# Performance work log

Hardware: AMD Instinct MI355X
Metric: run time of the kernel (lower is better)

## Reference

```python
import jax, jax.numpy as jnp
import numpy as np

N_QUBITS = 12
LAYERS = 8
N_CLASS = 10
BATCH = 2048
FEAT = 3072  # CIFAR-10 flattened 3*32*32
DIM = 2 ** N_QUBITS


def _apply_ry_layer(psi, angles):
    """Apply Ry(angles[q]) to qubit q for all q. psi: [B, 2,...,2] complex.
    kron order in the torch code makes qubit 0 the MSB -> tensor axis q+1."""
    c, s = jnp.cos(angles), jnp.sin(angles)
    for q in range(N_QUBITS):
        rot = jnp.stack([jnp.stack([c[q], -s[q]]), jnp.stack([s[q], c[q]])]).astype(psi.dtype)
        # contract qubit axis with rot (rows index output): psi'[..a..] = rot[a,b] psi[..b..]
        psi = jnp.moveaxis(jnp.tensordot(psi, rot, axes=([q + 1], [1])), -1, q + 1)
    return psi


def _cnot(psi, control, target):
    """CNOT == proj0(c) x I(t) + proj1(c) x X(t): flip target bit where control bit is 1."""
    ca, ta = control + 1, target + 1
    flipped = jnp.flip(psi, axis=ta)          # X on target qubit
    p0 = jax.lax.index_in_dim(psi, 0, axis=ca, keepdims=True)      # control = 0: identity
    p1 = jax.lax.index_in_dim(flipped, 1, axis=ca, keepdims=True)  # control = 1: X
    return jnp.concatenate([p0, p1], axis=ca)


def setup_inputs() -> dict:
    key = jax.random.key(0)
    kx, ka, kw = jax.random.split(key, 3)
    x = jax.random.normal(kx, (BATCH, FEAT), dtype=jnp.float32)
    angles = jax.random.uniform(ka, (LAYERS, N_QUBITS), minval=-0.01, maxval=0.01, dtype=jnp.float32)
    W = jax.random.normal(kw, (N_CLASS, DIM), dtype=jnp.float32) * np.float32(1.0 / np.sqrt(DIM))
    b = jnp.zeros((N_CLASS,), dtype=jnp.float32)
    return {"x": x, "angles": angles, "W": W, "b": b}


def reference(x, angles, W, b):
    B = x.shape[0]
    # CIFAR branch: right-pad features to 2^n, flatten (no-op for 2D), L2-normalize rows
    x = jnp.pad(x, ((0, 0), (0, DIM - x.shape[1])))
    x = x / jnp.linalg.norm(x, axis=1, keepdims=True)
    psi = x.astype(jnp.complex64).reshape((B,) + (2,) * N_QUBITS)
    for l in range(LAYERS):
        psi = _apply_ry_layer(psi, angles[l])
        # cx_linear_layer: CNOT(n-2,n-1), then CNOT(i,i+1) for i = n-3..0
        psi = _cnot(psi, N_QUBITS - 2, N_QUBITS - 1)
        for i in range(N_QUBITS - 3, -1, -1):
            psi = _cnot(psi, i, i + 1)
    probs = (psi.real ** 2 + psi.imag ** 2).reshape(B, DIM)  # Re(conj(psi)*psi)
    return probs @ W.T + b
```

## Files before the change

kernel.cpp:

```cpp
#include <hip/hip_runtime.h>
#include <math.h>

#define LAYERS  8
#define FEAT    3072
#define NCLASS  10
#define DIM     4096
#define ST      68
#define SBF     (ST * 64)

typedef float v2f __attribute__((ext_vector_type(2)));
typedef float v4f __attribute__((ext_vector_type(4)));

__device__ __forceinline__ int px6c(int r) {
    int u = r ^ (r >> 1); u ^= u >> 2; u ^= u >> 4; return u & 63;
}
__device__ __forceinline__ int gray6(int r) { return (r ^ (r >> 1)) & 63; }

__device__ __forceinline__ float getc(const v2f v[32], int u) {
    return (u & 1) ? v[u >> 1].y : v[u >> 1].x;
}
__device__ __forceinline__ void setc(v2f v[32], int u, float x) {
    if (u & 1) v[u >> 1].y = x; else v[u >> 1].x = x;
}
__device__ __forceinline__ float bpermf(int addr, float x) {
    return __int_as_float(__builtin_amdgcn_ds_bpermute(addr, __float_as_int(x)));
}

__device__ __forceinline__ void butterflies6(v2f v[32],
                                             const float* __restrict__ cl,
                                             const float* __restrict__ sl,
                                             int off) {
    {
        const float c = cl[off], s = sl[off];
        const v2f c2 = {c, c};
        const v2f ms = {-s, s};
#pragma unroll
        for (int i = 0; i < 32; ++i) {
            v2f a = v[i];
            v2f sw = {a.y, a.x};
            v[i] = a * c2 + sw * ms;
        }
    }
#pragma unroll
    for (int p = 1; p < 6; ++p) {
        const float c = cl[off - p], s = sl[off - p];
        const v2f c2 = {c, c};
        const v2f s2 = {s, s};
#pragma unroll
        for (int i0 = 0; i0 < 32; ++i0) {
            if (i0 & (1 << (p - 1))) continue;
            const int i1 = i0 | (1 << (p - 1));
            v2f a = v[i0], e = v[i1];
            v[i0] = a * c2 - e * s2;
            v[i1] = a * s2 + e * c2;
        }
    }
}

__device__ __forceinline__ void butterflies6_renamed(v2f v[32],
                                                     const float* __restrict__ cl,
                                                     const float* __restrict__ sl,
                                                     float psgn) {
    {
        const float c = cl[11], s = sl[11];
        const v2f c2 = {c, c};
        const v2f msA = {-s, s};
        const v2f msB = {s, -s};
#pragma unroll
        for (int k = 0; k < 32; ++k) {
            v2f a = v[k];
            v2f sw = {a.y, a.x};
            v[k] = a * c2 + sw * ((k & 1) ? msB : msA);
        }
    }
#pragma unroll
    for (int b = 1; b < 5; ++b) {
        const float c = cl[11 - b], s = sl[11 - b];
        const v2f c2 = {c, c};
#pragma unroll
        for (int m = 0; m < 32; ++m) {
            if (m & (1 << (b - 1))) continue;
            const int part = m ^ ((1 << b) - 1);
            const float sg = (m & (1 << b)) ? -s : s;
            const v2f sg2 = {sg, sg};
            const v2f A = v[m], E = v[part];
            const v2f Esw = {E.y, E.x};
            const v2f Asw = {A.y, A.x};
            v[m]    = A * c2 - Esw * sg2;
            v[part] = Asw * sg2 + E * c2;
        }
    }
    {
        const float c = cl[6];
        const float snl = psgn * sl[6];
        const v2f c2 = {c, c};
        const v2f sg2 = {snl, snl};
#pragma unroll
        for (int m = 0; m < 16; ++m) {
            const int part = m ^ 31;
            const v2f A = v[m], E = v[part];
            const v2f Esw = {E.y, E.x};
            const v2f Asw = {A.y, A.x};
            v[m]    = A * c2 - Esw * sg2;
            v[part] = Asw * sg2 + E * c2;
        }
    }
}

__global__ __launch_bounds__(64, 1)
void qnn_kernel(const float* __restrict__ x,
                const float* __restrict__ ang,
                const float* __restrict__ W,
                const float* __restrict__ bias,
                float* __restrict__ out,
                int batch)
{
    __shared__ __attribute__((aligned(16))) float lds[2 * SBF];
    __shared__ float cst[96], snt[96];

    const int t = threadIdx.x;
    const int b = blockIdx.x;
    const int b0 = 2 * b, b1 = 2 * b + 1;
    const bool has1 = (b1 < batch);

    {
        float a0 = ang[t];
        cst[t] = cosf(a0);
        snt[t] = sinf(a0);
        if (t < 32) {
            float a1 = ang[64 + t];
            cst[64 + t] = cosf(a1);
            snt[64 + t] = sinf(a1);
        }
    }

    v2f v0[32], v1[32];
    {
        const float* xb = x + (size_t)b0 * FEAT;
#pragma unroll
        for (int r = 0; r < 64; ++r) {
            if (r < FEAT / 64) setc(v0, r, xb[64 * r + t]);
            else               setc(v0, r, 0.f);
        }
    }
    if (has1) {
        const float* xb = x + (size_t)b1 * FEAT;
#pragma unroll
        for (int r = 0; r < 64; ++r) {
            if (r < FEAT / 64) setc(v1, r, xb[64 * r + t]);
            else               setc(v1, r, 0.f);
        }
    } else {
#pragma unroll
        for (int i = 0; i < 32; ++i) v1[i] = (v2f){0.f, 0.f};
    }

    float invn0, invn1;
    {
        v2f s2 = {0.f, 0.f};
#pragma unroll
        for (int i = 0; i < 32; ++i) s2 += v0[i] * v0[i];
        float ss = s2.x + s2.y;
#pragma unroll
        for (int o = 1; o < 64; o <<= 1) ss += __shfl_xor(ss, o, 64);
        invn0 = 1.0f / ss;
    }
    {
        v2f s2 = {0.f, 0.f};
#pragma unroll
        for (int i = 0; i < 32; ++i) s2 += v1[i] * v1[i];
        float ss = s2.x + s2.y;
#pragma unroll
        for (int o = 1; o < 64; o <<= 1) ss += __shfl_xor(ss, o, 64);
        invn1 = 1.0f / ss;
    }

    {
        const int slot = __builtin_amdgcn_s_getreg(4 | (4 << 6) | (1 << 11)) & 3;
#pragma unroll 1
        for (int i = 0; i < slot; ++i) __builtin_amdgcn_s_sleep(12);
    }

    int px = t ^ (t >> 1); px ^= px >> 2; px ^= px >> 4; px &= 63;
    const int A0 = 4 * px;
    const int A1 = 4 * (px ^ 63);
    const int u0 = t & 1;
    const float psgn = u0 ? -1.f : 1.f;
    const int gtl = gray6(t);
    const int bp  = gtl + 32 * ST * u0;
    const int bm  = gtl - 32 * ST * u0;

    auto storeRows = [&](const v2f* vv, const int SB) {
#pragma unroll
        for (int i = 0; i < 16; ++i) {
            v4f q = {vv[2 * i].x, vv[2 * i].y, vv[2 * i + 1].x, vv[2 * i + 1].y};
            *(v4f*)(lds + SB + ST * t + 4 * i) = q;
        }
    };
    auto readCols = [&](v2f* vv, const int SB) {
#pragma unroll
        for (int u = 0; u < 64; ++u)
            setc(vv, u, lds[SB + t + ST * u]);
    };
    auto foldedStore = [&](const v2f* vv, const int SB) {
#pragma unroll
        for (int s = 0; s < 64; ++s) {
            const int g = gray6(s);
            lds[SB + ((g & 32) ? bm : bp) + ST * g] = getc(vv, s);
        }
    };
    auto rowRead = [&](v2f* vv, const int SB) {
#pragma unroll
        for (int i = 0; i < 16; ++i) {
            v4f q = *(const v4f*)(lds + SB + ST * t + 4 * i);
            vv[2 * i]     = (v2f){q.x, q.y};
            vv[2 * i + 1] = (v2f){q.z, q.w};
        }
    };
    auto grayB = [&](v2f* vv) {
        float n[64];
#pragma unroll
        for (int r = 0; r < 64; ++r) {
            const int srcr = px6c(r);
            n[r] = bpermf((srcr & 1) ? A1 : A0, getc(vv, srcr));
        }
#pragma unroll
        for (int r = 0; r < 64; ++r) setc(vv, r, n[r]);
    };

    {
        const float* cl = cst;
        const float* sl = snt;
        butterflies6(v0, cl, sl, 5);
        butterflies6(v1, cl, sl, 5);
        storeRows(v0, 0);  storeRows(v1, SBF);
        readCols(v0, 0);   readCols(v1, SBF);
        butterflies6(v0, cl, sl, 11);
        butterflies6(v1, cl, sl, 11);
    }

#pragma unroll 1
    for (int p = 0; p < 4; ++p) {
        {
            const float* cl = cst + (2 * p + 1) * 12;
            const float* sl = snt + (2 * p + 1) * 12;

            butterflies6_renamed(v0, cl, sl, psgn);
            butterflies6_renamed(v1, cl, sl, psgn);
            foldedStore(v0, 0);  foldedStore(v1, SBF);
            rowRead(v0, 0);      rowRead(v1, SBF);
            butterflies6(v0, cl, sl, 5);
            butterflies6(v1, cl, sl, 5);

            if (p < 3) {
                grayB(v0);
                grayB(v1);
            }
        }

        if (p == 3) break;

        {
            const float* cl = cst + (2 * p + 2) * 12;
            const float* sl = snt + (2 * p + 2) * 12;

            butterflies6(v0, cl, sl, 5);
            butterflies6(v1, cl, sl, 5);
            storeRows(v0, 0);  storeRows(v1, SBF);
            readCols(v0, 0);   readCols(v1, SBF);
            butterflies6(v0, cl, sl, 11);
            butterflies6(v1, cl, sl, 11);
        }
    }

#pragma unroll
    for (int i = 0; i < 32; ++i) {
        const int g0 = 64 * gray6(2 * i);
        const int g1 = 64 * (gray6(2 * i) ^ 1);
        lds[g0 + gtl]        = v0[i].x * v0[i].x;
        lds[g1 + (gtl ^ 32)] = v0[i].y * v0[i].y;
        lds[SBF + g0 + gtl]        = v1[i].x * v1[i].x;
        lds[SBF + g1 + (gtl ^ 32)] = v1[i].y * v1[i].y;
    }

    float acc0[NCLASS], acc1[NCLASS];
#pragma unroll
    for (int c = 0; c < NCLASS; ++c) { acc0[c] = 0.f; acc1[c] = 0.f; }

#pragma unroll 1
    for (int k = 0; k < 16; ++k) {
        const v4f qa = *(const v4f*)(lds + 4 * t + 256 * k);
        const v4f qb = *(const v4f*)(lds + SBF + 4 * t + 256 * k);
        const float* wp = W + 4 * t + 256 * k;
#pragma unroll
        for (int c = 0; c < NCLASS; ++c) {
            const v4f w4 = *(const v4f*)(wp + c * DIM);
            acc0[c] += qa.x * w4.x + qa.y * w4.y + qa.z * w4.z + qa.w * w4.w;
            acc1[c] += qb.x * w4.x + qb.y * w4.y + qb.z * w4.z + qb.w * w4.w;
        }
    }

#pragma unroll
    for (int c = 0; c < NCLASS; ++c) {
        float a0 = acc0[c], a1 = acc1[c];
#pragma unroll
        for (int o = 1; o < 64; o <<= 1) {
            a0 += __shfl_xor(a0, o, 64);
            a1 += __shfl_xor(a1, o, 64);
        }
        if (t == 0) {
            out[b0 * NCLASS + c] = fmaf(a0, invn0, bias[c]);
            if (has1) out[b1 * NCLASS + c] = fmaf(a1, invn1, bias[c]);
        }
    }
}

extern "C" void kernel_launch(void* const* d_in, const int* in_sizes, int n_in,
                              void* d_out, int out_size, void* d_ws, size_t ws_size,
                              hipStream_t stream) {
    const float* x    = (const float*)d_in[0];
    const float* ang  = (const float*)d_in[1];
    const float* W    = (const float*)d_in[2];
    const float* bias = (const float*)d_in[3];
    float* out = (float*)d_out;
    const int batch = in_sizes[0] / FEAT;
    const int blocks = (batch + 1) / 2;
    qnn_kernel<<<blocks, 64, 0, stream>>>(x, ang, W, bias, out, batch);
}
```

Before: 122.2 us.

## Interleave LDS transposes of one state with butterflies of the other via packed FMA

Rewrites the butterfly stages with inline-asm v_pk_mul/v_pk_fma (including op_sel swap variants) so each complex rotation becomes one packed mul plus one packed fma. The two batch states' stages are then software-interleaved: LDS stores, reads and bpermute chunks for one state are issued alongside butterfly stages of the other. This is meant to hide LDS and cross-lane latency behind ALU work in a single-wave block. It raises register pressure (n0/n1 arrays live together), and inline asm limits compiler scheduling.

Result: slower. 131.3 us (+7.4%).

```diff
diff --git a/kernel.cpp b/kernel.cpp
--- a/kernel.cpp
+++ b/kernel.cpp
@@ -26,85 +26,73 @@
     return __int_as_float(__builtin_amdgcn_ds_bpermute(addr, __float_as_int(x)));
 }
 
-__device__ __forceinline__ void butterflies6(v2f v[32],
-                                             const float* __restrict__ cl,
-                                             const float* __restrict__ sl,
-                                             int off) {
-    {
-        const float c = cl[off], s = sl[off];
-        const v2f c2 = {c, c};
-        const v2f ms = {-s, s};
-#pragma unroll
-        for (int i = 0; i < 32; ++i) {
-            v2f a = v[i];
-            v2f sw = {a.y, a.x};
-            v[i] = a * c2 + sw * ms;
-        }
-    }
-#pragma unroll
-    for (int p = 1; p < 6; ++p) {
-        const float c = cl[off - p], s = sl[off - p];
-        const v2f c2 = {c, c};
-        const v2f s2 = {s, s};
-#pragma unroll
-        for (int i0 = 0; i0 < 32; ++i0) {
-            if (i0 & (1 << (p - 1))) continue;
-            const int i1 = i0 | (1 << (p - 1));
-            v2f a = v[i0], e = v[i1];
-            v[i0] = a * c2 - e * s2;
-            v[i1] = a * s2 + e * c2;
-        }
-    }
-}
-
-__device__ __forceinline__ void butterflies6_renamed(v2f v[32],
-                                                     const float* __restrict__ cl,
-                                                     const float* __restrict__ sl,
-                                                     float psgn) {
-    {
-        const float c = cl[11], s = sl[11];
-        const v2f c2 = {c, c};
-        const v2f msA = {-s, s};
-        const v2f msB = {s, -s};
-#pragma unroll
-        for (int k = 0; k < 32; ++k) {
-            v2f a = v[k];
-            v2f sw = {a.y, a.x};
-            v[k] = a * c2 + sw * ((k & 1) ? msB : msA);
-        }
-    }
-#pragma unroll
-    for (int b = 1; b < 5; ++b) {
-        const float c = cl[11 - b], s = sl[11 - b];
-        const v2f c2 = {c, c};
-#pragma unroll
-        for (int m = 0; m < 32; ++m) {
-            if (m & (1 << (b - 1))) continue;
-            const int part = m ^ ((1 << b) - 1);
-            const float sg = (m & (1 << b)) ? -s : s;
-            const v2f sg2 = {sg, sg};
-            const v2f A = v[m], E = v[part];
-            const v2f Esw = {E.y, E.x};
-            const v2f Asw = {A.y, A.x};
-            v[m]    = A * c2 - Esw * sg2;
-            v[part] = Asw * sg2 + E * c2;
-        }
-    }
-    {
-        const float c = cl[6];
-        const float snl = psgn * sl[6];
-        const v2f c2 = {c, c};
-        const v2f sg2 = {snl, snl};
-#pragma unroll
-        for (int m = 0; m < 16; ++m) {
-            const int part = m ^ 31;
-            const v2f A = v[m], E = v[part];
-            const v2f Esw = {E.y, E.x};
-            const v2f Asw = {A.y, A.x};
-            v[m]    = A * c2 - Esw * sg2;
-            v[part] = Asw * sg2 + E * c2;
-        }
-    }
+__device__ __forceinline__ v2f pk_mul(v2f a, v2f b) {
+    v2f d; asm("v_pk_mul_f32 %0, %1, %2" : "=v"(d) : "v"(a), "v"(b)); return d;
+}
+__device__ __forceinline__ v2f pk_fma(v2f a, v2f b, v2f c) {
+    v2f d; asm("v_pk_fma_f32 %0, %1, %2, %3" : "=v"(d) : "v"(a), "v"(b), "v"(c)); return d;
+}
+__device__ __forceinline__ v2f pk_fma_swap(v2f a, v2f b, v2f c) {
+    v2f d; asm("v_pk_fma_f32 %0, %1, %2, %3 op_sel:[1,0,0] op_sel_hi:[0,1,1]"
+               : "=v"(d) : "v"(a), "v"(b), "v"(c));
+    return d;
+}
+
+__device__ __forceinline__ void bf_s0(v2f v[32], float c, float s) {
+    const v2f c2 = {c, c}, ms = {-s, s};
+#pragma unroll
+    for (int i = 0; i < 32; ++i) {
+        v2f a = v[i];
+        v[i] = pk_fma_swap(a, ms, pk_mul(a, c2));
+    }
+}
+__device__ __forceinline__ void bf_sp(v2f v[32], int p, float c, float s) {
+    const v2f c2 = {c, c}, s2 = {s, s}, ns2 = {-s, -s};
+#pragma unroll
+    for (int i0 = 0; i0 < 32; ++i0) {
+        if (i0 & (1 << (p - 1))) continue;
+        const int i1 = i0 | (1 << (p - 1));
+        v2f a = v[i0], e = v[i1];
+        v[i0] = pk_fma(e, ns2, pk_mul(a, c2));
+        v[i1] = pk_fma(a, s2,  pk_mul(e, c2));
+    }
+}
+__device__ __forceinline__ void bfr_s0(v2f v[32], float c, float s) {
+    const v2f c2 = {c, c}, msA = {-s, s}, msB = {s, -s};
+#pragma unroll
+    for (int k = 0; k < 32; ++k) {
+        v2f a = v[k];
+        v[k] = pk_fma_swap(a, (k & 1) ? msB : msA, pk_mul(a, c2));
+    }
+}
+__device__ __forceinline__ void bfr_sb(v2f v[32], int b, float c, float s) {
+    const v2f c2 = {c, c};
+#pragma unroll
+    for (int m = 0; m < 32; ++m) {
+        if (m & (1 << (b - 1))) continue;
+        const int part = m ^ ((1 << b) - 1);
+        const float sg = (m & (1 << b)) ? -s : s;
+        const v2f sg2 = {sg, sg}, nsg2 = {-sg, -sg};
+        v2f A = v[m], E = v[part];
+        v[m]    = pk_fma_swap(E, nsg2, pk_mul(A, c2));
+        v[part] = pk_fma_swap(A, sg2,  pk_mul(E, c2));
+    }
+}
+__device__ __forceinline__ void bfr_s5(v2f v[32], float c, float snl) {
+    const v2f c2 = {c, c}, sg2 = {snl, snl}, nsg2 = {-snl, -snl};
+#pragma unroll
+    for (int m = 0; m < 16; ++m) {
+        const int part = m ^ 31;
+        v2f A = v[m], E = v[part];
+        v[m]    = pk_fma_swap(E, nsg2, pk_mul(A, c2));
+        v[part] = pk_fma_swap(A, sg2,  pk_mul(E, c2));
+    }
+}
+__device__ __forceinline__ void bf6_full(v2f v[32], const float* __restrict__ cl,
+                                         const float* __restrict__ sl, int off) {
+    bf_s0(v, cl[off], sl[off]);
+#pragma unroll
+    for (int p = 1; p < 6; ++p) bf_sp(v, p, cl[off - p], sl[off - p]);
 }
 
 __global__ __launch_bounds__(64, 1)
@@ -159,7 +147,7 @@
     {
         v2f s2 = {0.f, 0.f};
 #pragma unroll
-        for (int i = 0; i < 32; ++i) s2 += v0[i] * v0[i];
+        for (int i = 0; i < 32; ++i) s2 = pk_fma(v0[i], v0[i], s2);
         float ss = s2.x + s2.y;
 #pragma unroll
         for (int o = 1; o < 64; o <<= 1) ss += __shfl_xor(ss, o, 64);
@@ -168,7 +156,7 @@
     {
         v2f s2 = {0.f, 0.f};
 #pragma unroll
-        for (int i = 0; i < 32; ++i) s2 += v1[i] * v1[i];
+        for (int i = 0; i < 32; ++i) s2 = pk_fma(v1[i], v1[i], s2);
         float ss = s2.x + s2.y;
 #pragma unroll
         for (int o = 1; o < 64; o <<= 1) ss += __shfl_xor(ss, o, 64);
@@ -190,40 +178,40 @@
     const int bp  = gtl + 32 * ST * u0;
     const int bm  = gtl - 32 * ST * u0;
 
-    auto storeRows = [&](const v2f* vv, const int SB) {
-#pragma unroll
-        for (int i = 0; i < 16; ++i) {
+    auto stR = [&](const v2f* vv, const int SB, int i0, int i1) {
+#pragma unroll
+        for (int i = i0; i < i1; ++i) {
             v4f q = {vv[2 * i].x, vv[2 * i].y, vv[2 * i + 1].x, vv[2 * i + 1].y};
             *(v4f*)(lds + SB + ST * t + 4 * i) = q;
         }
     };
-    auto readCols = [&](v2f* vv, const int SB) {
-#pragma unroll
-        for (int u = 0; u < 64; ++u)
-            setc(vv, u, lds[SB + t + ST * u]);
-    };
-    auto foldedStore = [&](const v2f* vv, const int SB) {
-#pragma unroll
-        for (int s = 0; s < 64; ++s) {
+    auto rdC = [&](v2f* vv, const int SB, int u0c, int u1c) {
+#pragma unroll
+        for (int u = u0c; u < u1c; ++u) setc(vv, u, lds[SB + t + ST * u]);
+    };
+    auto fS = [&](const v2f* vv, const int SB, int s0, int s1) {
+#pragma unroll
+        for (int s = s0; s < s1; ++s) {
             const int g = gray6(s);
             lds[SB + ((g & 32) ? bm : bp) + ST * g] = getc(vv, s);
         }
     };
-    auto rowRead = [&](v2f* vv, const int SB) {
-#pragma unroll
-        for (int i = 0; i < 16; ++i) {
+    auto rR = [&](v2f* vv, const int SB, int i0, int i1) {
+#pragma unroll
+        for (int i = i0; i < i1; ++i) {
             v4f q = *(const v4f*)(lds + SB + ST * t + 4 * i);
             vv[2 * i]     = (v2f){q.x, q.y};
             vv[2 * i + 1] = (v2f){q.z, q.w};
         }
     };
-    auto grayB = [&](v2f* vv) {
-        float n[64];
-#pragma unroll
-        for (int r = 0; r < 64; ++r) {
-            const int srcr = px6c(r);
-            n[r] = bpermf((srcr & 1) ? A1 : A0, getc(vv, srcr));
-        }
+    auto gG = [&](const v2f* vv, float* n, int r0, int r1) {
+#pragma unroll
+        for (int r = r0; r < r1; ++r) {
+            const int sr = px6c(r);
+            n[r] = bpermf((sr & 1) ? A1 : A0, getc(vv, sr));
+        }
+    };
+    auto gA = [&](v2f* vv, const float* n) {
 #pragma unroll
         for (int r = 0; r < 64; ++r) setc(vv, r, n[r]);
     };
@@ -231,45 +219,85 @@
     {
         const float* cl = cst;
         const float* sl = snt;
-        butterflies6(v0, cl, sl, 5);
-        butterflies6(v1, cl, sl, 5);
-        storeRows(v0, 0);  storeRows(v1, SBF);
-        readCols(v0, 0);   readCols(v1, SBF);
-        butterflies6(v0, cl, sl, 11);
-        butterflies6(v1, cl, sl, 11);
+        bf6_full(v0, cl, sl, 5);
+        stR(v0, 0, 0, 16);     bf_s0(v1, cl[5], sl[5]);
+        rdC(v0, 0, 0, 13);     bf_sp(v1, 1, cl[4], sl[4]);
+        rdC(v0, 0, 13, 26);    bf_sp(v1, 2, cl[3], sl[3]);
+        rdC(v0, 0, 26, 39);    bf_sp(v1, 3, cl[2], sl[2]);
+        rdC(v0, 0, 39, 52);    bf_sp(v1, 4, cl[1], sl[1]);
+        rdC(v0, 0, 52, 64);    bf_sp(v1, 5, cl[0], sl[0]);
+        stR(v1, SBF, 0, 16);   bf_s0(v0, cl[11], sl[11]);
+        rdC(v1, SBF, 0, 13);   bf_sp(v0, 1, cl[10], sl[10]);
+        rdC(v1, SBF, 13, 26);  bf_sp(v0, 2, cl[9],  sl[9]);
+        rdC(v1, SBF, 26, 39);  bf_sp(v0, 3, cl[8],  sl[8]);
+        rdC(v1, SBF, 39, 52);  bf_sp(v0, 4, cl[7],  sl[7]);
+        rdC(v1, SBF, 52, 64);  bf_sp(v0, 5, cl[6],  sl[6]);
+        bf6_full(v1, cl, sl, 11);
     }
 
 #pragma unroll 1
     for (int p = 0; p < 4; ++p) {
-        {
-            const float* cl = cst + (2 * p + 1) * 12;
-            const float* sl = snt + (2 * p + 1) * 12;
-
-            butterflies6_renamed(v0, cl, sl, psgn);
-            butterflies6_renamed(v1, cl, sl, psgn);
-            foldedStore(v0, 0);  foldedStore(v1, SBF);
-            rowRead(v0, 0);      rowRead(v1, SBF);
-            butterflies6(v0, cl, sl, 5);
-            butterflies6(v1, cl, sl, 5);
-
-            if (p < 3) {
-                grayB(v0);
-                grayB(v1);
-            }
-        }
-
-        if (p == 3) break;
-
-        {
-            const float* cl = cst + (2 * p + 2) * 12;
-            const float* sl = snt + (2 * p + 2) * 12;
-
-            butterflies6(v0, cl, sl, 5);
-            butterflies6(v1, cl, sl, 5);
-            storeRows(v0, 0);  storeRows(v1, SBF);
-            readCols(v0, 0);   readCols(v1, SBF);
-            butterflies6(v0, cl, sl, 11);
-            butterflies6(v1, cl, sl, 11);
+        float n0[64], n1[64];
+        const float* cl = cst + (2 * p + 1) * 12;
+        const float* sl = snt + (2 * p + 1) * 12;
+        const float snl = psgn * sl[6];
+
+        bfr_s0(v0, cl[11], sl[11]);
+        bfr_sb(v0, 1, cl[10], sl[10]);
+        bfr_sb(v0, 2, cl[9],  sl[9]);
+        bfr_sb(v0, 3, cl[8],  sl[8]);
+        bfr_sb(v0, 4, cl[7],  sl[7]);
+        bfr_s5(v0, cl[6], snl);
+        fS(v0, 0, 0, 14);      bfr_s0(v1, cl[11], sl[11]);
+        fS(v0, 0, 14, 28);     bfr_sb(v1, 1, cl[10], sl[10]);
+        fS(v0, 0, 28, 42);     bfr_sb(v1, 2, cl[9],  sl[9]);
+        fS(v0, 0, 42, 56);     bfr_sb(v1, 3, cl[8],  sl[8]);
+        fS(v0, 0, 56, 64);
+        rR(v0, 0, 0, 3);       bfr_sb(v1, 4, cl[7],  sl[7]);
+        rR(v0, 0, 3, 10);      bfr_s5(v1, cl[6], snl);
+        rR(v0, 0, 10, 16);
+        fS(v1, SBF, 0, 14);    bf_s0(v0, cl[5], sl[5]);
+        fS(v1, SBF, 14, 28);   bf_sp(v0, 1, cl[4], sl[4]);
+        fS(v1, SBF, 28, 42);   bf_sp(v0, 2, cl[3], sl[3]);
+        fS(v1, SBF, 42, 56);   bf_sp(v0, 3, cl[2], sl[2]);
+        fS(v1, SBF, 56, 64);
+        rR(v1, SBF, 0, 3);     bf_sp(v0, 4, cl[1], sl[1]);
+        rR(v1, SBF, 3, 10);    bf_sp(v0, 5, cl[0], sl[0]);
+        rR(v1, SBF, 10, 16);
+
+        if (p < 3) {
+            gG(v0, n0, 0, 11);     bf_s0(v1, cl[5], sl[5]);
+            gG(v0, n0, 11, 22);    bf_sp(v1, 1, cl[4], sl[4]);
+            gG(v0, n0, 22, 33);    bf_sp(v1, 2, cl[3], sl[3]);
+            gG(v0, n0, 33, 44);    bf_sp(v1, 3, cl[2], sl[2]);
+            gG(v0, n0, 44, 55);    bf_sp(v1, 4, cl[1], sl[1]);
+            gG(v0, n0, 55, 64);    bf_sp(v1, 5, cl[0], sl[0]);
+            gA(v0, n0);
+
+            const float* cle = cst + (2 * p + 2) * 12;
+            const float* sle = snt + (2 * p + 2) * 12;
+            gG(v1, n1, 0, 11);     bf_s0(v0, cle[5], sle[5]);
+            gG(v1, n1, 11, 22);    bf_sp(v0, 1, cle[4], sle[4]);
+            gG(v1, n1, 22, 33);    bf_sp(v0, 2, cle[3], sle[3]);
+            gG(v1, n1, 33, 44);    bf_sp(v0, 3, cle[2], sle[2]);
+            gG(v1, n1, 44, 55);    bf_sp(v0, 4, cle[1], sle[1]);
+            gG(v1, n1, 55, 64);    bf_sp(v0, 5, cle[0], sle[0]);
+            gA(v1, n1);
+            stR(v0, 0, 0, 16);     bf_s0(v1, cle[5], sle[5]);
+            rdC(v0, 0, 0, 13);     bf_sp(v1, 1, cle[4], sle[4]);
+            rdC(v0, 0, 13, 26);    bf_sp(v1, 2, cle[3], sle[3]);
+            rdC(v0, 0, 26, 39);    bf_sp(v1, 3, cle[2], sle[2]);
+            rdC(v0, 0, 39, 52);    bf_sp(v1, 4, cle[1], sle[1]);
+            rdC(v0, 0, 52, 64);    bf_sp(v1, 5, cle[0], sle[0]);
+            stR(v1, SBF, 0, 16);   bf_s0(v0, cle[11], sle[11]);
+            rdC(v1, SBF, 0, 13);   bf_sp(v0, 1, cle[10], sle[10]);
+            rdC(v1, SBF, 13, 26);  bf_sp(v0, 2, cle[9],  sle[9]);
+            rdC(v1, SBF, 26, 39);  bf_sp(v0, 3, cle[8],  sle[8]);
+            rdC(v1, SBF, 39, 52);  bf_sp(v0, 4, cle[7],  sle[7]);
+            rdC(v1, SBF, 52, 64);  bf_sp(v0, 5, cle[6],  sle[6]);
+            bf6_full(v1, cle, sle, 11);
+        } else {
+            bf6_full(v1, cl, sl, 5);
         }
     }
 
```
